# Performance work log

Hardware: AMD Instinct MI355X
Metric: run time of the kernel (lower is better)

## Reference

```python
import jax, jax.numpy as jnp
import numpy as np

B = 4096
HASH_BITS = 128
TEACHER_DIM = 768
TEMPERATURE = 0.2
CONTRASTIVE_W = 1.0
DISTILL_W = 0.5
QUANT_W = 0.01


def _l2_normalize(x, eps=1e-12):
    # matches torch F.normalize(dim=-1)
    n = jnp.sqrt(jnp.sum(x * x, axis=-1, keepdims=True))
    return x / jnp.maximum(n, eps)


def setup_inputs() -> dict:
    key = jax.random.key(0)
    k1, k2, k3, k4 = jax.random.split(key, 4)
    logits = jax.random.normal(k1, (B, HASH_BITS), dtype=jnp.float32)
    # binary {-1,+1} codes as in the module contract
    hash_codes = jnp.sign(jax.random.normal(k2, (B, HASH_BITS), dtype=jnp.float32))
    hash_codes = jnp.where(hash_codes == 0, 1.0, hash_codes)
    teacher_embed = jax.random.normal(k3, (B, TEACHER_DIM), dtype=jnp.float32)
    # sparse random positives plus self-positives (guarantees each row nonempty)
    rand_pos = jax.random.uniform(k4, (B, B)) < 0.002
    eye = jnp.eye(B, dtype=bool)
    positive_mask = rand_pos | eye
    return {
        "logits": logits,
        "hash_codes": hash_codes,
        "teacher_embed": teacher_embed,
        "positive_mask": positive_mask,
    }


def reference(logits, hash_codes, teacher_embed, positive_mask):
    teacher = _l2_normalize(teacher_embed)

    # ---- contrastive (vectorized form of the per-row python loop) ----
    ln = _l2_normalize(logits)
    sim = (ln @ ln.T) / TEMPERATURE  # [B, B]
    eye = jnp.eye(sim.shape[0], dtype=bool)
    sim_masked = jnp.where(eye, -jnp.inf, sim)
    # per-row stable logsumexp over self-masked similarities
    log_denom = jax.nn.logsumexp(sim_masked, axis=1)  # [B]
    pm = positive_mask.astype(sim.dtype)
    cnt = pm.sum(axis=1)  # [B]
    pos_mean = (sim * pm).sum(axis=1) / jnp.maximum(cnt, 1.0)
    has_pos = cnt > 0
    per_row = jnp.where(has_pos, -pos_mean + log_denom, 0.0)
    num_pos = jnp.maximum(has_pos.sum(), 1)
    loss_cont = per_row.sum() / num_pos.astype(sim.dtype)

    # ---- distillation: hash similarity vs teacher similarity MSE ----
    hash_sim = (hash_codes @ hash_codes.T) / hash_codes.shape[-1]
    teacher_sim = teacher @ teacher.T
    loss_distill = jnp.mean((hash_sim - teacher_sim) ** 2)

    # ---- quantization: push |logits| toward 1 ----
    loss_quant = jnp.mean(jnp.abs(jnp.abs(logits) - 1.0))

    total = (
        CONTRASTIVE_W * loss_cont
        + DISTILL_W * loss_distill
        + QUANT_W * loss_quant
    )
    return total
```

## Files before the change

kernel.cpp:

```cpp
#include <hip/hip_runtime.h>


typedef unsigned short u16x8 __attribute__((ext_vector_type(8)));
typedef __bf16 bf16x8 __attribute__((ext_vector_type(8)));
typedef float f32x4 __attribute__((ext_vector_type(4)));

__device__ __forceinline__ unsigned short f2bf(float f) {
  union { float f; unsigned int u; } v; v.f = f;
  unsigned int u = v.u;
  return (unsigned short)((u + 0x7FFFu + ((u >> 16) & 1u)) >> 16);
}

__global__ __launch_bounds__(256) void prep(const float* __restrict__ logits,
                                            const float* __restrict__ hash,
                                            const float* __restrict__ teacher,
                                            unsigned short* __restrict__ P,
                                            float* __restrict__ qpart,
                                            float* __restrict__ rowexp,
                                            float* __restrict__ possum,
                                            float* __restrict__ cntw,
                                            float* __restrict__ dtot) {
  const int r = blockIdx.x * 4 + (threadIdx.x >> 6);
  const int lane = threadIdx.x & 63;
  float tv[12];
  float ss = 0.f;
#pragma unroll
  for (int i = 0; i < 12; ++i) {
    tv[i] = teacher[(size_t)r * 768 + i * 64 + lane];
    ss += tv[i] * tv[i];
  }
  const float l0 = logits[(size_t)r * 128 + lane];
  const float l1 = logits[(size_t)r * 128 + 64 + lane];
  const float h0 = hash[(size_t)r * 128 + lane];
  const float h1 = hash[(size_t)r * 128 + 64 + lane];
  float ssl = l0 * l0 + l1 * l1;
  float qv = fabsf(fabsf(l0) - 1.f) + fabsf(fabsf(l1) - 1.f);
#pragma unroll
  for (int off = 1; off < 64; off <<= 1) {
    ss += __shfl_xor(ss, off, 64);
    ssl += __shfl_xor(ssl, off, 64);
    qv += __shfl_xor(qv, off, 64);
  }
  const float rnt = 1.f / fmaxf(sqrtf(ss), 1e-12f);
  const float rnl = 1.f / fmaxf(sqrtf(ssl), 1e-12f);
  unsigned short* Pr = P + (size_t)r * 1024;
  Pr[lane] = f2bf(l0 * rnl);
  Pr[64 + lane] = f2bf(l1 * rnl);
  Pr[128 + lane] = f2bf(h0 * 0.08838834764831845f);
  Pr[192 + lane] = f2bf(h1 * 0.08838834764831845f);
#pragma unroll
  for (int i = 0; i < 12; ++i) Pr[256 + i * 64 + lane] = f2bf(tv[i] * rnt);
  if (lane == 0) {
    qpart[r] = qv;
    rowexp[r] = 0.f; possum[r] = 0.f; cntw[r] = 0.f;
    if (r == 0) *dtot = 0.f;
  }
}

#define STAGE64(COL0)                                                          \
  {                                                                            \
    _Pragma("unroll") for (int it = 0; it < 4; ++it) {                         \
      const int task = it * 256 + t;                                           \
      const int row = task >> 3;                                               \
      const int g = (task & 7) ^ (row & 7);                                    \
      const unsigned short* gpA =                                              \
          P + (size_t)(ti + row) * 1024 + (COL0) + g * 8;                      \
      __builtin_amdgcn_global_load_lds(                                        \
          (const __attribute__((address_space(1))) void*)gpA,                  \
          (__attribute__((address_space(3))) void*)&S[it * 2048 + wave * 512], \
          16, 0, 0);                                                           \
      if (offdiag) {                                                           \
        const unsigned short* gpB =                                            \
            P + (size_t)(tj + row) * 1024 + (COL0) + g * 8;                    \
        __builtin_amdgcn_global_load_lds(                                      \
            (const __attribute__((address_space(1))) void*)gpB,                \
            (__attribute__((address_space(3)))                                 \
                 void*)&S[8192 + it * 2048 + wave * 512],                      \
            16, 0, 0);                                                         \
      }                                                                        \
    }                                                                          \
  }

#define MFMA_CHUNK()                                                           \
  {                                                                            \
    _Pragma("unroll") for (int ks = 0; ks < 2; ++ks) {                         \
      bf16x8 af[4], bfr[4];                                                    \
      _Pragma("unroll") for (int rt = 0; rt < 4; ++rt) {                       \
        const int ar = wy * 64 + rt * 16 + l15;                                \
        af[rt] =                                                               \
            *(const bf16x8*)&S[ar * 64 + ((ks * 4 + qd) ^ (l15 & 7)) * 8];     \
      }                                                                        \
      _Pragma("unroll") for (int ct = 0; ct < 4; ++ct) {                       \
        const int br = wx * 64 + ct * 16 + l15;                                \
        bfr[ct] = *(const bf16x8*)&S[boff + br * 64 +                          \
                                     ((ks * 4 + qd) ^ (l15 & 7)) * 8];         \
      }                                                                        \
      _Pragma("unroll") for (int rt = 0; rt < 4; ++rt)                         \
          _Pragma("unroll") for (int ct = 0; ct < 4; ++ct) acc[rt][ct] =       \
          __builtin_amdgcn_mfma_f32_16x16x32_bf16(af[rt], bfr[ct],             \
                                                  acc[rt][ct], 0, 0, 0);       \
    }                                                                          \
  }

__global__ __launch_bounds__(256, 3) void mega(const unsigned short* __restrict__ P,
                                               const void* __restrict__ mask,
                                               float* __restrict__ rowexp,
                                               float* __restrict__ possum,
                                               float* __restrict__ cntw,
                                               float* __restrict__ dtot) {
  __shared__ __align__(16) unsigned short S[16384];
  __shared__ float redrow[128][2], redcol[128][2], red4[4];

  const int t = threadIdx.x;
  const int wave = t >> 6, lane = t & 63;
  const int qd = lane >> 4, l15 = lane & 15;
  const int wy = wave >> 1, wx = wave & 1;

  const int b = (int)blockIdx.x;
  const bool isD = (b & 1) == 0;
  const int bb = b >> 1;
  const int l = (bb & 7) * 66 + (bb >> 3);
  int bi = (int)((65.0f - sqrtf(4225.0f - 8.0f * (float)l)) * 0.5f);
  while (bi * (65 - bi) / 2 > l) --bi;
  while ((bi + 1) * (64 - bi) / 2 <= l) ++bi;
  const int bj = bi + (l - bi * (65 - bi) / 2);
  const int ti = bi * 128, tj = bj * 128;
  const bool offdiag = (bi != bj);
  const int boff = offdiag ? 8192 : 0;

  f32x4 acc[4][4];
#pragma unroll
  for (int rt = 0; rt < 4; ++rt)
#pragma unroll
    for (int ct = 0; ct < 4; ++ct) acc[rt][ct] = {0.f, 0.f, 0.f, 0.f};

  if (isD) {
    for (int kc = 0; kc < 14; ++kc) {
      const int col0 = (kc < 12) ? (256 + kc * 64) : (128 + (kc - 12) * 64);
      __syncthreads();
      STAGE64(col0);
      __syncthreads();
      if (kc == 12) {
#pragma unroll
        for (int rt = 0; rt < 4; ++rt)
#pragma unroll
          for (int ct = 0; ct < 4; ++ct) acc[rt][ct] = -acc[rt][ct];
      }
      MFMA_CHUNK();
    }
    float dsum = 0.f;
#pragma unroll
    for (int rt = 0; rt < 4; ++rt)
#pragma unroll
      for (int ct = 0; ct < 4; ++ct)
#pragma unroll
        for (int i = 0; i < 4; ++i) dsum += acc[rt][ct][i] * acc[rt][ct][i];
#pragma unroll
    for (int off = 1; off < 64; off <<= 1) dsum += __shfl_xor(dsum, off, 64);
    if (lane == 0) red4[wave] = dsum;
    __syncthreads();
    if (t == 0)
      atomicAdd(dtot, (offdiag ? 2.0f : 1.0f) *
                          (red4[0] + red4[1] + red4[2] + red4[3]));
  } else {
    for (int kc = 0; kc < 2; ++kc) {
      const int col0 = kc * 64;
      __syncthreads();
      STAGE64(col0);
      __syncthreads();
      MFMA_CHUNK();
    }

    __syncthreads();
    unsigned char* MD = (unsigned char*)S;
    unsigned char* MM = (unsigned char*)S + 16384;
    const bool is_byte = ((const unsigned char*)mask)[4097] != 0;
    if (is_byte) {
      const unsigned char* m8 = (const unsigned char*)mask;
#pragma unroll
      for (int it = 0; it < 4; ++it) {
        const int task = it * 256 + t;
        const int row = task >> 3, seg = task & 7;
        *(uint4*)&MD[row * 128 + seg * 16] =
            *(const uint4*)&m8[(size_t)(ti + row) * 4096 + tj + seg * 16];
        if (offdiag)
          *(uint4*)&MM[row * 128 + seg * 16] =
              *(const uint4*)&m8[(size_t)(tj + row) * 4096 + ti + seg * 16];
      }
    } else {
      const unsigned int* m32 = (const unsigned int*)mask;
#pragma unroll
      for (int it = 0; it < 16; ++it) {
        const int task = it * 256 + t;
        const int row = task >> 5, seg = task & 31;
        uint4 v = *(const uint4*)&m32[(size_t)(ti + row) * 4096 + tj + seg * 4];
        uchar4 pk;
        pk.x = v.x ? 1 : 0; pk.y = v.y ? 1 : 0;
        pk.z = v.z ? 1 : 0; pk.w = v.w ? 1 : 0;
        *(uchar4*)&MD[row * 128 + seg * 4] = pk;
        if (offdiag) {
          uint4 w = *(const uint4*)&m32[(size_t)(tj + row) * 4096 + ti + seg * 4];
          uchar4 pm;
          pm.x = w.x ? 1 : 0; pm.y = w.y ? 1 : 0;
          pm.z = w.z ? 1 : 0; pm.w = w.w ? 1 : 0;
          *(uchar4*)&MM[row * 128 + seg * 4] = pm;
        }
      }
    }
    __syncthreads();

    float colp[4] = {0.f, 0.f, 0.f, 0.f};
#pragma unroll
    for (int rt = 0; rt < 4; ++rt) {
#pragma unroll
      for (int r = 0; r < 4; ++r) {
        const int mrow = wy * 64 + rt * 16 + qd * 4 + r;
        const int m = ti + mrow;
        float se = 0.f;
#pragma unroll
        for (int ct = 0; ct < 4; ++ct) {
          const int ncol = wx * 64 + ct * 16 + l15;
          const int n = tj + ncol;
          const float sim = acc[rt][ct][r] * 5.0f;
          const float e = __expf(sim);
          if (offdiag || mrow != ncol) se += e;
          if (offdiag) colp[ct] += e;
          if (MD[mrow * 128 + ncol]) {
            atomicAdd(&possum[m], sim);
            atomicAdd(&cntw[m], 1.0f);
          }
          if (offdiag && MM[ncol * 128 + mrow]) {
            atomicAdd(&possum[n], sim);
            atomicAdd(&cntw[n], 1.0f);
          }
        }
#pragma unroll
        for (int off = 1; off < 16; off <<= 1) se += __shfl_xor(se, off, 64);
        if (l15 == 0) redrow[mrow][wx] = se;
      }
    }
    if (offdiag) {
#pragma unroll
      for (int ct = 0; ct < 4; ++ct) {
        float ce = colp[ct];
        ce += __shfl_xor(ce, 16, 64);
        ce += __shfl_xor(ce, 32, 64);
        if (qd == 0) redcol[wx * 64 + ct * 16 + l15][wy] = ce;
      }
    }
    __syncthreads();
    if (t < 128) {
      atomicAdd(&rowexp[ti + t], redrow[t][0] + redrow[t][1]);
      if (offdiag) atomicAdd(&rowexp[tj + t], redcol[t][0] + redcol[t][1]);
    }
  }
}

__global__ __launch_bounds__(1024) void finalize(const float* __restrict__ rowexp,
                                                 const float* __restrict__ possum,
                                                 const float* __restrict__ cnt,
                                                 const float* __restrict__ qpart,
                                                 const float* __restrict__ dtot,
                                                 float* __restrict__ out) {
  const int t = threadIdx.x;
  const int wave = t >> 6, lane = t & 63;
  float c = 0.f, q = 0.f;
  for (int m = t; m < 4096; m += 1024) {
    c += logf(rowexp[m]) - possum[m] / fmaxf(cnt[m], 1.0f);
    q += qpart[m];
  }
#pragma unroll
  for (int off = 1; off < 64; off <<= 1) {
    c += __shfl_xor(c, off, 64);
    q += __shfl_xor(q, off, 64);
  }
  __shared__ float sc[16], sq[16];
  if (lane == 0) { sc[wave] = c; sq[wave] = q; }
  __syncthreads();
  if (t == 0) {
    float C = 0.f, Q = 0.f;
    for (int i = 0; i < 16; ++i) { C += sc[i]; Q += sq[i]; }
    out[0] = C * (1.0f / 4096.0f) + 0.5f * (dtot[0] * (1.0f / 16777216.0f)) +
             0.01f * (Q * (1.0f / 524288.0f));
  }
}

extern "C" void kernel_launch(void* const* d_in, const int* in_sizes, int n_in,
                              void* d_out, int out_size, void* d_ws, size_t ws_size,
                              hipStream_t stream) {
  const float* logits = (const float*)d_in[0];
  const float* hash = (const float*)d_in[1];
  const float* teacher = (const float*)d_in[2];
  const void* mask = d_in[3];
  float* out = (float*)d_out;

  char* ws = (char*)d_ws;
  float* rowexp = (float*)(ws + 0);
  float* possum = (float*)(ws + 16384);
  float* cntw = (float*)(ws + 32768);
  float* qpart = (float*)(ws + 49152);
  float* dtot = (float*)(ws + 65536);
  unsigned short* P = (unsigned short*)(ws + 98304);

  prep<<<1024, 256, 0, stream>>>(logits, hash, teacher, P, qpart, rowexp,
                                 possum, cntw, dtot);
  mega<<<1056, 256, 0, stream>>>(P, mask, rowexp, possum, cntw, dtot);
  finalize<<<1, 1024, 0, stream>>>(rowexp, possum, cntw, qpart, dtot, out);
}
```

Measured before the change: 173.7 us.

## Double-buffer LDS staging in mega kernel and schedule distill blocks first

Shared memory is doubled so the global-to-LDS load of the next K chunk is issued before the MFMA work on the current chunk. This replaces the two barriers per chunk with one and hides load latency behind the math. The block index mapping now places all 528 distillation tiles (14 chunks each) before the contrastive tiles instead of interleaving them, so the long blocks start first. The larger LDS footprint lowers the occupancy hint from 3 to 2 blocks per CU, which reduces the latency hiding that came from having more resident waves.

```diff
diff --git a/kernel.cpp b/kernel.cpp
--- a/kernel.cpp
+++ b/kernel.cpp
@@ -57,7 +57,7 @@
   }
 }
 
-#define STAGE64(COL0)                                                          \
+#define STAGE64(COL0, BUF)                                                     \
   {                                                                            \
     _Pragma("unroll") for (int it = 0; it < 4; ++it) {                         \
       const int task = it * 256 + t;                                           \
@@ -67,7 +67,8 @@
           P + (size_t)(ti + row) * 1024 + (COL0) + g * 8;                      \
       __builtin_amdgcn_global_load_lds(                                        \
           (const __attribute__((address_space(1))) void*)gpA,                  \
-          (__attribute__((address_space(3))) void*)&S[it * 2048 + wave * 512], \
+          (__attribute__((address_space(3)))                                   \
+               void*)&S[(BUF) * 16384 + it * 2048 + wave * 512],               \
           16, 0, 0);                                                           \
       if (offdiag) {                                                           \
         const unsigned short* gpB =                                            \
@@ -75,24 +76,25 @@
         __builtin_amdgcn_global_load_lds(                                      \
             (const __attribute__((address_space(1))) void*)gpB,                \
             (__attribute__((address_space(3)))                                 \
-                 void*)&S[8192 + it * 2048 + wave * 512],                      \
+                 void*)&S[(BUF) * 16384 + 8192 + it * 2048 + wave * 512],      \
             16, 0, 0);                                                         \
       }                                                                        \
     }                                                                          \
   }
 
-#define MFMA_CHUNK()                                                           \
+#define MFMA_CHUNK(BUF)                                                        \
   {                                                                            \
+    const int sb = (BUF) * 16384;                                              \
     _Pragma("unroll") for (int ks = 0; ks < 2; ++ks) {                         \
       bf16x8 af[4], bfr[4];                                                    \
       _Pragma("unroll") for (int rt = 0; rt < 4; ++rt) {                       \
         const int ar = wy * 64 + rt * 16 + l15;                                \
-        af[rt] =                                                               \
-            *(const bf16x8*)&S[ar * 64 + ((ks * 4 + qd) ^ (l15 & 7)) * 8];     \
+        af[rt] = *(const bf16x8*)&S[sb + ar * 64 +                             \
+                                    ((ks * 4 + qd) ^ (l15 & 7)) * 8];          \
       }                                                                        \
       _Pragma("unroll") for (int ct = 0; ct < 4; ++ct) {                       \
         const int br = wx * 64 + ct * 16 + l15;                                \
-        bfr[ct] = *(const bf16x8*)&S[boff + br * 64 +                          \
+        bfr[ct] = *(const bf16x8*)&S[sb + boff + br * 64 +                     \
                                      ((ks * 4 + qd) ^ (l15 & 7)) * 8];         \
       }                                                                        \
       _Pragma("unroll") for (int rt = 0; rt < 4; ++rt)                         \
@@ -102,13 +104,13 @@
     }                                                                          \
   }
 
-__global__ __launch_bounds__(256, 3) void mega(const unsigned short* __restrict__ P,
+__global__ __launch_bounds__(256, 2) void mega(const unsigned short* __restrict__ P,
                                                const void* __restrict__ mask,
                                                float* __restrict__ rowexp,
                                                float* __restrict__ possum,
                                                float* __restrict__ cntw,
                                                float* __restrict__ dtot) {
-  __shared__ __align__(16) unsigned short S[16384];
+  __shared__ __align__(16) unsigned short S[32768];
   __shared__ float redrow[128][2], redcol[128][2], red4[4];
 
   const int t = threadIdx.x;
@@ -117,8 +119,8 @@
   const int wy = wave >> 1, wx = wave & 1;
 
   const int b = (int)blockIdx.x;
-  const bool isD = (b & 1) == 0;
-  const int bb = b >> 1;
+  const bool isD = b < 528;
+  const int bb = isD ? b : b - 528;
   const int l = (bb & 7) * 66 + (bb >> 3);
   int bi = (int)((65.0f - sqrtf(4225.0f - 8.0f * (float)l)) * 0.5f);
   while (bi * (65 - bi) / 2 > l) --bi;
@@ -135,18 +137,23 @@
     for (int ct = 0; ct < 4; ++ct) acc[rt][ct] = {0.f, 0.f, 0.f, 0.f};
 
   if (isD) {
+    STAGE64(256, 0);
+    __syncthreads();
+#pragma unroll
     for (int kc = 0; kc < 14; ++kc) {
-      const int col0 = (kc < 12) ? (256 + kc * 64) : (128 + (kc - 12) * 64);
+      if (kc < 13) {
+        const int nc = kc + 1;
+        const int col1 = (nc < 12) ? (256 + nc * 64) : (128 + (nc - 12) * 64);
+        STAGE64(col1, (nc & 1));
+      }
+      if (kc == 12) {
+#pragma unroll
+        for (int rt = 0; rt < 4; ++rt)
+#pragma unroll
+          for (int ct = 0; ct < 4; ++ct) acc[rt][ct] = -acc[rt][ct];
+      }
+      MFMA_CHUNK(kc & 1);
       __syncthreads();
-      STAGE64(col0);
-      __syncthreads();
-      if (kc == 12) {
-#pragma unroll
-        for (int rt = 0; rt < 4; ++rt)
-#pragma unroll
-          for (int ct = 0; ct < 4; ++ct) acc[rt][ct] = -acc[rt][ct];
-      }
-      MFMA_CHUNK();
     }
     float dsum = 0.f;
 #pragma unroll
@@ -163,15 +170,13 @@
       atomicAdd(dtot, (offdiag ? 2.0f : 1.0f) *
                           (red4[0] + red4[1] + red4[2] + red4[3]));
   } else {
-    for (int kc = 0; kc < 2; ++kc) {
-      const int col0 = kc * 64;
-      __syncthreads();
-      STAGE64(col0);
-      __syncthreads();
-      MFMA_CHUNK();
-    }
-
-    __syncthreads();
+    STAGE64(0, 0);
+    __syncthreads();
+    STAGE64(64, 1);
+    MFMA_CHUNK(0);
+    __syncthreads();
+    MFMA_CHUNK(1);
+
     unsigned char* MD = (unsigned char*)S;
     unsigned char* MM = (unsigned char*)S + 16384;
     const bool is_byte = ((const unsigned char*)mask)[4097] != 0;
```

Result: slower. 182.3 us (+4.9%).
